# Kernel tuning notes

Hardware: AMD Instinct MI355X
Metric: run time of the kernel (lower is better)

Reference implementation:

```python
import jax, jax.numpy as jnp
import numpy as np

B, X_DIM, Y_DIM, T, LAT, H1, CH = 4096, 128, 64, 200, 100, 100, 50


def setup_inputs() -> dict:
    key = jax.random.key(0)
    ks = jax.random.split(key, 16)

    def rn(k, shape, scale):
        return (jax.random.normal(k, shape) * scale).astype(jnp.float32)

    def lin(k, fin, fout):
        # weight stored [in, out] so forward is x @ W + b (same math as torch Linear)
        return rn(k, (fin, fout), 1.0 / np.sqrt(fin)), jnp.zeros((fout,), jnp.float32)

    Wmu1, bmu1 = lin(ks[0], X_DIM, H1)
    Wmu2, bmu2 = lin(ks[1], H1, LAT)
    Wsig1, bsig1 = lin(ks[2], X_DIM, H1)
    Wsig2, bsig2 = lin(ks[3], H1, LAT)
    Wih, bih = lin(ks[4], 2 * Y_DIM, 3 * LAT)   # GRUCell input weights (r|z|n)
    Whh, bhh = lin(ks[5], LAT, 3 * LAT)          # GRUCell hidden weights (r|z|n)
    Wl1, bl1 = lin(ks[6], LAT, LAT)
    Wl2, bl2 = lin(ks[7], LAT, Y_DIM)
    Wc1, bc1 = lin(ks[8], LAT, CH)
    Wc2, bc2 = lin(ks[9], CH, 1)

    return dict(
        x=jax.random.normal(ks[10], (B, X_DIM), jnp.float32),
        y=jax.random.normal(ks[11], (B, Y_DIM, T), jnp.float32),
        y_mask=jax.random.bernoulli(ks[12], 0.5, (B, Y_DIM, T)),
        Wmu1=Wmu1, bmu1=bmu1, Wmu2=Wmu2, bmu2=bmu2,
        Wsig1=Wsig1, bsig1=bsig1, Wsig2=Wsig2, bsig2=bsig2,
        Wih=Wih, bih=bih, Whh=Whh, bhh=bhh,
        Wl1=Wl1, bl1=bl1, Wl2=Wl2, bl2=bl2,
        Wc1=Wc1, bc1=bc1, Wc2=Wc2, bc2=bc2,
    )


def reference(x, y, y_mask,
              Wmu1, bmu1, Wmu2, bmu2,
              Wsig1, bsig1, Wsig2, bsig2,
              Wih, bih, Whh, bhh,
              Wl1, bl1, Wl2, bl2,
              Wc1, bc1, Wc2, bc2):
    Bb, ydim, Tt = y.shape
    # initial hidden state: eval-mode reparametrize returns mu (log_std unused)
    mu0 = jnp.tanh(x @ Wmu1 + bmu1) @ Wmu2 + bmu2          # [B, LAT]
    h0 = mu0

    y_seq = jnp.moveaxis(y, 2, 0)                            # [T, B, ydim]
    m_seq = jnp.moveaxis(y_mask, 2, 0)                       # [T, B, ydim] bool

    def step(carry, tm):
        h, y_prev = carry
        y_t, m_t = tm
        # teacher forcing: observed entries from y, rest from previous prediction
        y_in = jnp.where(m_t, y_t, y_prev)                   # [B, ydim]
        mf = m_t.astype(h.dtype)
        # interleave (value, mask) per feature -> [B, 2*ydim]
        x_il = jnp.stack([y_in, mf], axis=2).reshape(Bb, 2 * ydim)
        gx = x_il @ Wih + bih                                # [B, 3*LAT]
        gh = h @ Whh + bhh
        gx_r, gx_z, gx_n = jnp.split(gx, 3, axis=1)
        gh_r, gh_z, gh_n = jnp.split(gh, 3, axis=1)
        r = jax.nn.sigmoid(gx_r + gh_r)
        z = jax.nn.sigmoid(gx_z + gh_z)
        n = jnp.tanh(gx_n + r * gh_n)
        h_new = (1.0 - z) * n + z * h                        # torch GRUCell update
        out_t = jnp.tanh(h_new @ Wl1 + bl1) @ Wl2 + bl2      # [B, ydim]
        return (h_new, out_t), out_t

    init = (h0, jnp.zeros((Bb, ydim), h0.dtype))
    (h_T, _), outs = jax.lax.scan(step, init, (y_seq, m_seq))
    output = jnp.moveaxis(outs, 0, 2)                        # [B, ydim, T]
    out_class = jax.nn.sigmoid(jax.nn.relu(h_T @ Wc1 + bc1) @ Wc2 + bc2)[:, 0]
    return output, out_class
```

## Files before the change

### kernel.cpp

```cpp
#include <hip/hip_runtime.h>
#include <hip/hip_bf16.h>


#define BSZ   4096
#define XD    128
#define YD    64
#define TT    200
#define NH3   300
#define RPB   16
#define NBLK  (BSZ / RPB)

typedef unsigned short u16;
typedef unsigned int   u32;
typedef __attribute__((ext_vector_type(8))) short s16x8;
typedef __attribute__((ext_vector_type(4))) float f32x4;

__device__ __forceinline__ float bf_lo(u32 u){ return __uint_as_float(u << 16); }
__device__ __forceinline__ float bf_hi(u32 u){ return __uint_as_float(u & 0xFFFF0000u); }
__device__ __forceinline__ u16 f2bf(float f){
  u32 u = __float_as_uint(f);
  u32 r = (u + 0x7FFFu + ((u >> 16) & 1u)) >> 16;
  return (u16)r;
}
__device__ __forceinline__ float loadf(const void* p, size_t i, int fmode){
  return (fmode == 0) ? __uint_as_float(((u32)((const u16*)p)[i]) << 16)
                      : ((const float*)p)[i];
}
__device__ __forceinline__ float fsig(float x){ return 1.f/(1.f + __expf(-x)); }
__device__ __forceinline__ float ftanh(float x){ float e = __expf(2.f*x); return 1.f - 2.f/(e + 1.f); }

__device__ __forceinline__ f32x4 mfma16(uint4 a, uint4 b, f32x4 c){
  s16x8 as, bs;
  __builtin_memcpy(&as, &a, 16);
  __builtin_memcpy(&bs, &b, 16);
  return __builtin_amdgcn_mfma_f32_16x16x32_bf16(as, bs, c, 0, 0, 0);
}

__device__ __forceinline__ float dotblk(const float* xr, const u16* wb, int n, int N, int KB){
  float a = 0.f;
  const uint4* wp = (const uint4*)wb;
  #pragma unroll
  for (int kb = 0; kb < KB; ++kb){
    uint4 u = wp[kb * N + n];
    const float4* xp = (const float4*)(xr + (kb << 3));
    float4 x0 = xp[0], x1 = xp[1];
    a += x0.x*bf_lo(u.x) + x0.y*bf_hi(u.x) + x0.z*bf_lo(u.y) + x0.w*bf_hi(u.y);
    a += x1.x*bf_lo(u.z) + x1.y*bf_hi(u.z) + x1.z*bf_lo(u.w) + x1.w*bf_hi(u.w);
  }
  return a;
}

__global__ void detect_kernel(const void* mask, const void* x, int* flags){
  __shared__ int cnt[4];
  if (threadIdx.x < 4) cnt[threadIdx.x] = 0;
  __syncthreads();
  if (blockIdx.x == 0){
    const unsigned char* p = (const unsigned char*)mask;
    int c0=0, c1=0, c2=0, c3=0;
    for (int i = threadIdx.x; i < 4096; i += 256){
      unsigned char b = p[i];
      if (b == 0x3F && (i & 3) == 1) c0++;
      if (b == 0x3F && (i & 3) == 3) c1++;
      if (b == 1    && (i & 3) != 0) c2++;
      if (b == 1)                    c3++;
    }
    atomicAdd(&cnt[0], c0); atomicAdd(&cnt[1], c1);
    atomicAdd(&cnt[2], c2); atomicAdd(&cnt[3], c3);
    __syncthreads();
    if (threadIdx.x == 0){
      int mm;
      if      (cnt[0] > 0) mm = 0;
      else if (cnt[1] > 0) mm = 1;
      else if (cnt[2] > 0) mm = 3;
      else if (cnt[3] > 0) mm = 2;
      else                 mm = 0;
      flags[1] = mm;
    }
  } else {
    const u16* u = (const u16*)x;
    int c = 0;
    for (int i = threadIdx.x; i < 4096; i += 256){
      int ex = (u[i] >> 7) & 0xFF;
      if (ex >= 147) c++;
    }
    atomicAdd(&cnt[0], c);
    __syncthreads();
    if (threadIdx.x == 0) flags[0] = (cnt[0] > 32) ? 1 : 0;
  }
}

struct WtP { const void* src[3]; u16* dst[3]; const int* flags; };

__global__ void wtrans_kernel(WtP a){
  const int Ks[3]  = {128, 100, 100};
  const int Ns[3]  = {100, 100,  50};
  const int KBs[3] = { 16,  13,  13};
  int m   = blockIdx.x >> 3;
  int sub = blockIdx.x & 7;
  int K = Ks[m], N = Ns[m], KB = KBs[m];
  const void* src = a.src[m];
  u16* dst = a.dst[m];
  int fmode = a.flags[0];
  int E = KB * N * 8;
  for (int e = sub*256 + threadIdx.x; e < E; e += 8*256){
    int idx = e >> 3, kc = e & 7;
    int n = idx % N, kb = idx / N;
    int k = kb*8 + kc;
    float v = (k < K) ? loadf(src, (size_t)k * N + n, fmode) : 0.f;
    dst[e] = f2bf(v);
  }
}

struct FrP { const void* src[4]; u16* dst[4]; const int* flags; };

__global__ void fragk(FrP a){
  const int Ks[4]  = {128, 100, 100, 100};
  const int Ns[4]  = {300, 300, 100,  64};
  const int NTs[4] = { 20,  20,   8,   4};
  int m   = blockIdx.x >> 3;
  int sub = blockIdx.x & 7;
  int K = Ks[m], N = Ns[m];
  const void* src = a.src[m];
  u16* dst = a.dst[m];
  int fmode = a.flags[0];
  int E = NTs[m] * 2048;
  for (int e = sub*256 + threadIdx.x; e < E; e += 8*256){
    int j    = e & 7;
    int lane = (e >> 3) & 63;
    int kc   = (e >> 9) & 3;
    int nt   = e >> 11;
    int k = kc*32 + ((lane >> 4) << 3) + j;
    int n = nt*16 + (lane & 15);
    float v = (k < K && n < N) ? loadf(src, (size_t)k * N + n, fmode) : 0.f;
    dst[e] = f2bf(v);
  }
}

struct MainP {
  const void *x, *y, *mask;
  const void *bmu1, *bmu2, *bih, *bhh, *bl1, *bl2, *bc1, *bc2, *wc2;
  const u16 *Wmu1b, *Wmu2b, *Wc1b;
  const u16 *fih, *fhh, *fl1, *fl2;
  const int* flags;
  void* out;
};

__device__ __forceinline__ void load_win8(const void* Y, const void* M, int row0, int t,
                                          int fmode, int mmode, uint4* yv, u32& mb){
  mb = 0u;
  #pragma unroll
  for (int p = 0; p < 4; ++p){
    int idx = threadIdx.x + (p << 8);
    int r = idx >> 6, d = idx & 63;
    size_t base = ((size_t)(row0 + r)*64 + d)*200 + t;
    uint4 yw;
    if (fmode == 0){
      yw = *(const uint4*)((const u16*)Y + base);
    } else {
      const float* yf = (const float*)Y + base;
      float4 f0 = *(const float4*)yf;
      float4 f1 = *(const float4*)(yf + 4);
      yw.x = (u32)f2bf(f0.x) | ((u32)f2bf(f0.y) << 16);
      yw.y = (u32)f2bf(f0.z) | ((u32)f2bf(f0.w) << 16);
      yw.z = (u32)f2bf(f1.x) | ((u32)f2bf(f1.y) << 16);
      yw.w = (u32)f2bf(f1.z) | ((u32)f2bf(f1.w) << 16);
    }
    yv[p] = yw;
    u32 bits = 0;
    if (mmode == 0){
      uint4 mw = *(const uint4*)((const u16*)M + base);
      u32 w0 = mw.x, w1 = mw.y, w2 = mw.z, w3 = mw.w;
      if (w0 & 0xFFFFu) bits |= 1u;  if (w0 >> 16) bits |= 2u;
      if (w1 & 0xFFFFu) bits |= 4u;  if (w1 >> 16) bits |= 8u;
      if (w2 & 0xFFFFu) bits |= 16u; if (w2 >> 16) bits |= 32u;
      if (w3 & 0xFFFFu) bits |= 64u; if (w3 >> 16) bits |= 128u;
    } else if (mmode == 1){
      const float* mf = (const float*)M + base;
      float4 f0 = *(const float4*)mf;
      float4 f1 = *(const float4*)(mf + 4);
      if (f0.x != 0.f) bits |= 1u;  if (f0.y != 0.f) bits |= 2u;
      if (f0.z != 0.f) bits |= 4u;  if (f0.w != 0.f) bits |= 8u;
      if (f1.x != 0.f) bits |= 16u; if (f1.y != 0.f) bits |= 32u;
      if (f1.z != 0.f) bits |= 64u; if (f1.w != 0.f) bits |= 128u;
    } else if (mmode == 2){
      const int* mi = (const int*)M + base;
      int4 v0 = *(const int4*)mi;
      int4 v1 = *(const int4*)(mi + 4);
      if (v0.x) bits |= 1u;  if (v0.y) bits |= 2u;
      if (v0.z) bits |= 4u;  if (v0.w) bits |= 8u;
      if (v1.x) bits |= 16u; if (v1.y) bits |= 32u;
      if (v1.z) bits |= 64u; if (v1.w) bits |= 128u;
    } else {
      uint2 u = *(const uint2*)((const unsigned char*)M + base);
      #pragma unroll
      for (int q = 0; q < 4; ++q){
        if ((u.x >> (q*8)) & 0xFFu) bits |= 1u << q;
        if ((u.y >> (q*8)) & 0xFFu) bits |= 1u << (4 + q);
      }
    }
    mb |= bits << (p << 3);
  }
}

__global__ __launch_bounds__(256, 1) void gru_main(MainP P){
  __shared__ u16   XIL[RPB*136];
  __shared__ u16   HB [RPB*136];
  __shared__ u16   HN2[RPB*136];
  __shared__ float HF [RPB*108];
  __shared__ float SRZ[RPB*204];
  __shared__ float GXN[RPB*108];
  __shared__ float GHN[RPB*108];
  __shared__ u16   OS [RPB*64*16];
  __shared__ float BIH[304], BHH[304], BL1[128], BL2[64], BC1[64], WC2[64], BMU1[112], BMU2[112];

  const int tid  = threadIdx.x;
  const int row0 = blockIdx.x * RPB;
  const int fmode = P.flags[0];
  const int mmode = P.flags[1];
  const int w  = tid >> 6;
  const int ln = tid & 63;
  const int col = ln & 15;
  const int q4  = (ln >> 4) << 2;

  uint4 yc[4], yn[4];
  u32 mc, mn;
  load_win8(P.y, P.mask, row0, 0, fmode, mmode, yc, mc);
  load_win8(P.y, P.mask, row0, 8, fmode, mmode, yn, mn);

  uint4 wih[5][4], whh[5][4], wl1[2][4], wl2[4];
  #pragma unroll
  for (int i = 0; i < 5; ++i){
    int nt = w + 4*i;
    #pragma unroll
    for (int kc = 0; kc < 4; ++kc){
      wih[i][kc] = *(const uint4*)(P.fih + (((nt*4 + kc) << 6) + ln)*8);
      whh[i][kc] = *(const uint4*)(P.fhh + (((nt*4 + kc) << 6) + ln)*8);
    }
  }
  #pragma unroll
  for (int i = 0; i < 2; ++i){
    int nt = w + 4*i;
    #pragma unroll
    for (int kc = 0; kc < 4; ++kc)
      wl1[i][kc] = *(const uint4*)(P.fl1 + (((nt*4 + kc) << 6) + ln)*8);
  }
  #pragma unroll
  for (int kc = 0; kc < 4; ++kc)
    wl2[kc] = *(const uint4*)(P.fl2 + (((w*4 + kc) << 6) + ln)*8);

  for (int i = tid; i < RPB*136/2; i += 256){ ((u32*)HB)[i] = 0u; ((u32*)HN2)[i] = 0u; }
  for (int i = tid; i < RPB*108;   i += 256){ HF[i] = 0.f; GXN[i] = 0.f; GHN[i] = 0.f; }
  for (int i = tid; i < RPB*64*8;  i += 256){ ((u32*)OS)[i] = 0u; }

  for (int i = tid; i < 304; i += 256){
    BIH[i] = (i < 300) ? loadf(P.bih, i, fmode) : 0.f;
    BHH[i] = (i < 300) ? loadf(P.bhh, i, fmode) : 0.f;
  }
  if (tid < 128) BL1[tid] = (tid < 100) ? loadf(P.bl1, tid, fmode) : 0.f;
  if (tid < 64){
    BL2[tid] = loadf(P.bl2, tid, fmode);
    BC1[tid] = (tid < 50) ? loadf(P.bc1, tid, fmode) : 0.f;
    WC2[tid] = (tid < 50) ? loadf(P.wc2, tid, fmode) : 0.f;
  }
  if (tid < 112){
    BMU1[tid] = (tid < 100) ? loadf(P.bmu1, tid, fmode) : 0.f;
    BMU2[tid] = (tid < 100) ? loadf(P.bmu2, tid, fmode) : 0.f;
  }
  __syncthreads();

  #pragma unroll
  for (int p = 0; p < 2; ++p){
    int idx = tid + (p << 8);
    int r = idx >> 5, kq = idx & 31;
    size_t base = ((size_t)(row0 + r) << 7) + ((size_t)kq << 2);
    float v0, v1, v2, v3;
    if (fmode == 0){
      uint2 u = *(const uint2*)((const u16*)P.x + base);
      v0 = bf_lo(u.x); v1 = bf_hi(u.x); v2 = bf_lo(u.y); v3 = bf_hi(u.y);
    } else {
      float4 f = *(const float4*)((const float*)P.x + base);
      v0 = f.x; v1 = f.y; v2 = f.z; v3 = f.w;
    }
    float* dst = &SRZ[r*204 + (kq << 2)];
    dst[0] = v0; dst[1] = v1; dst[2] = v2; dst[3] = v3;
  }
  __syncthreads();
  for (int p = 0; p < 7; ++p){
    int idx = tid + (p << 8);
    if (idx < RPB*100){
      int r = idx / 100, j = idx - r*100;
      GXN[r*108 + j] = ftanh(BMU1[j] + dotblk(&SRZ[r*204], P.Wmu1b, j, 100, 16));
    }
  }
  __syncthreads();
  for (int p = 0; p < 7; ++p){
    int idx = tid + (p << 8);
    if (idx < RPB*100){
      int r = idx / 100, j = idx - r*100;
      float hv = BMU2[j] + dotblk(&GXN[r*108], P.Wmu2b, j, 100, 13);
      HF[r*108 + j] = hv;
      HB[r*136 + j] = f2bf(hv);
    }
  }
  __syncthreads();

  for (int t = 0; t < TT; ++t){
    const int tc8 = t & 7;

    if (tc8 == 0 && t){
      #pragma unroll
      for (int p = 0; p < 4; ++p) yc[p] = yn[p];
      mc = mn;
      if (t + 8 < TT) load_win8(P.y, P.mask, row0, t + 8, fmode, mmode, yn, mn);
    }
    if ((t & 15) == 0 && t){
      int t0 = t - 16;
      #pragma unroll
      for (int p = 0; p < 4; ++p){
        int idx = tid + (p << 8);
        int r = idx >> 6, d = idx & 63;
        size_t base = ((size_t)(row0 + r)*64 + d)*200 + t0;
        const uint4* po = (const uint4*)&OS[(r*64 + d)*16];
        if (fmode == 0){
          u16* ob = (u16*)P.out + base;
          *(uint4*)ob = po[0];
          *(uint4*)(ob + 8) = po[1];
        } else {
          float* of = (float*)P.out + base;
          uint4 a = po[0], b = po[1];
          float4 f0 = {bf_lo(a.x), bf_hi(a.x), bf_lo(a.y), bf_hi(a.y)};
          float4 f1 = {bf_lo(a.z), bf_hi(a.z), bf_lo(a.w), bf_hi(a.w)};
          float4 f2 = {bf_lo(b.x), bf_hi(b.x), bf_lo(b.y), bf_hi(b.y)};
          float4 f3 = {bf_lo(b.z), bf_hi(b.z), bf_lo(b.w), bf_hi(b.w)};
          *(float4*)of = f0; *(float4*)(of+4) = f1;
          *(float4*)(of+8) = f2; *(float4*)(of+12) = f3;
        }
      }
    }

    #pragma unroll
    for (int p = 0; p < 4; ++p){
      int idx = tid + (p << 8);
      int r = idx >> 6, d = idx & 63;
      u32 w01 = (tc8 & 2) ? yc[p].y : yc[p].x;
      u32 w23 = (tc8 & 2) ? yc[p].w : yc[p].z;
      u32 word = (tc8 & 4) ? w23 : w01;
      u16 yv16 = (tc8 & 1) ? (u16)(word >> 16) : (u16)(word & 0xFFFFu);
      bool mv = (mc >> ((p << 3) | tc8)) & 1u;
      u16 yp16 = OS[(r*64 + d)*16 + ((t + 15) & 15)];
      u32 val = (u32)(mv ? yv16 : yp16) | ((mv ? 0x3F80u : 0u) << 16);
      *(u32*)(&XIL[r*136 + (d << 1)]) = val;
    }
    __syncthreads();

    {
      uint4 xa[4], ha[4];
      #pragma unroll
      for (int kc = 0; kc < 4; ++kc){
        int ao = (ln & 15)*136 + kc*32 + ((ln >> 4) << 3);
        xa[kc] = *(const uint4*)(&XIL[ao]);
        ha[kc] = *(const uint4*)(&HB[ao]);
      }
      #pragma unroll
      for (int i = 0; i < 3; ++i){
        f32x4 ac = {0.f, 0.f, 0.f, 0.f};
        #pragma unroll
        for (int kc = 0; kc < 4; ++kc) ac = mfma16(xa[kc], wih[i][kc], ac);
        #pragma unroll
        for (int kc = 0; kc < 4; ++kc) ac = mfma16(ha[kc], whh[i][kc], ac);
        int n = (w + 4*i)*16 + col;
        float bb = BIH[n] + BHH[n];
        #pragma unroll
        for (int reg = 0; reg < 4; ++reg)
          SRZ[(q4 + reg)*204 + n] = ac[reg] + bb;
      }
      #pragma unroll
      for (int i = 3; i < 5; ++i){
        f32x4 ax = {0.f,0.f,0.f,0.f}, ah = {0.f,0.f,0.f,0.f};
        #pragma unroll
        for (int kc = 0; kc < 4; ++kc){
          ax = mfma16(xa[kc], wih[i][kc], ax);
          ah = mfma16(ha[kc], whh[i][kc], ah);
        }
        int n = (w + 4*i)*16 + col;
        if (n < 200){
          float bb = BIH[n] + BHH[n];
          #pragma unroll
          for (int reg = 0; reg < 4; ++reg)
            SRZ[(q4 + reg)*204 + n] = ax[reg] + ah[reg] + bb;
        } else if (n < 304){
          float b1 = BIH[n], b2 = BHH[n];
          #pragma unroll
          for (int reg = 0; reg < 4; ++reg){
            GXN[(q4 + reg)*108 + n - 200] = ax[reg] + b1;
            GHN[(q4 + reg)*108 + n - 200] = ah[reg] + b2;
          }
        }
      }
    }
    __syncthreads();

    for (int p = 0; p < 7; ++p){
      int idx = tid + (p << 8);
      if (idx < RPB*100){
        int r = idx / 100, j = idx - r*100;
        float rr = fsig(SRZ[r*204 + j]);
        float zz = fsig(SRZ[r*204 + 100 + j]);
        float nn = ftanh(GXN[r*108 + j] + rr*GHN[r*108 + j]);
        float hv = (1.f - zz)*nn + zz*HF[r*108 + j];
        HF[r*108 + j] = hv;
        HB[r*136 + j] = f2bf(hv);
      }
    }
    __syncthreads();

    {
      uint4 ha[4];
      #pragma unroll
      for (int kc = 0; kc < 4; ++kc){
        int ao = (ln & 15)*136 + kc*32 + ((ln >> 4) << 3);
        ha[kc] = *(const uint4*)(&HB[ao]);
      }
      #pragma unroll
      for (int i = 0; i < 2; ++i){
        f32x4 ac = {0.f,0.f,0.f,0.f};
        #pragma unroll
        for (int kc = 0; kc < 4; ++kc) ac = mfma16(ha[kc], wl1[i][kc], ac);
        int n = (w + 4*i)*16 + col;
        #pragma unroll
        for (int reg = 0; reg < 4; ++reg)
          HN2[(q4 + reg)*136 + n] = f2bf(ftanh(ac[reg] + BL1[n]));
      }
    }
    __syncthreads();

    {
      uint4 na[4];
      #pragma unroll
      for (int kc = 0; kc < 4; ++kc){
        int ao = (ln & 15)*136 + kc*32 + ((ln >> 4) << 3);
        na[kc] = *(const uint4*)(&HN2[ao]);
      }
      f32x4 ac = {0.f,0.f,0.f,0.f};
      #pragma unroll
      for (int kc = 0; kc < 4; ++kc) ac = mfma16(na[kc], wl2[kc], ac);
      int d = w*16 + col;
      #pragma unroll
      for (int reg = 0; reg < 4; ++reg){
        float o = ac[reg] + BL2[d];
        OS[((q4 + reg)*64 + d)*16 + (t & 15)] = f2bf(o);
      }
    }
    __syncthreads();
  }

  {
    int t0 = TT - 8;
    #pragma unroll
    for (int p = 0; p < 4; ++p){
      int idx = tid + (p << 8);
      int r = idx >> 6, d = idx & 63;
      size_t base = ((size_t)(row0 + r)*64 + d)*200 + t0;
      const uint4* po = (const uint4*)&OS[(r*64 + d)*16];
      if (fmode == 0){
        *(uint4*)((u16*)P.out + base) = po[0];
      } else {
        float* of = (float*)P.out + base;
        uint4 a = po[0];
        float4 f0 = {bf_lo(a.x), bf_hi(a.x), bf_lo(a.y), bf_hi(a.y)};
        float4 f1 = {bf_lo(a.z), bf_hi(a.z), bf_lo(a.w), bf_hi(a.w)};
        *(float4*)of = f0; *(float4*)(of+4) = f1;
      }
    }
  }

  for (int p = 0; p < 4; ++p){
    int idx = tid + (p << 8);
    if (idx < RPB*50){
      int r = idx / 50, j = idx - r*50;
      float c = BC1[j] + dotblk(&HF[r*108], P.Wc1b, j, 50, 13);
      GXN[r*108 + j] = fmaxf(c, 0.f);
    }
  }
  __syncthreads();
  if (tid < RPB){
    float oc = loadf(P.bc2, 0, fmode);
    for (int j = 0; j < 50; ++j) oc += GXN[tid*108 + j]*WC2[j];
    float sg = fsig(oc);
    size_t off = (size_t)BSZ*YD*TT + row0 + tid;
    if (fmode == 0) ((u16*)P.out)[off] = f2bf(sg);
    else            ((float*)P.out)[off] = sg;
  }
}

extern "C" void kernel_launch(void* const* d_in, const int* in_sizes, int n_in,
                              void* d_out, int out_size, void* d_ws, size_t ws_size,
                              hipStream_t stream){
  int* flags = (int*)d_ws;
  u16* wb = (u16*)((char*)d_ws + 256);
  u16* Wmu1b = wb;
  u16* Wmu2b = wb + 12800;
  u16* Wc1b  = wb + 23200;
  u16* fih   = wb + 28400;
  u16* fhh   = wb + 69360;
  u16* fl1   = wb + 110320;
  u16* fl2   = wb + 126704;

  detect_kernel<<<2, 256, 0, stream>>>(d_in[2], d_in[0], flags);

  WtP wp;
  wp.flags = flags;
  wp.src[0] = d_in[3];  wp.dst[0] = Wmu1b;
  wp.src[1] = d_in[5];  wp.dst[1] = Wmu2b;
  wp.src[2] = d_in[19]; wp.dst[2] = Wc1b;
  wtrans_kernel<<<24, 256, 0, stream>>>(wp);

  FrP fp;
  fp.flags = flags;
  fp.src[0] = d_in[11]; fp.dst[0] = fih;
  fp.src[1] = d_in[13]; fp.dst[1] = fhh;
  fp.src[2] = d_in[15]; fp.dst[2] = fl1;
  fp.src[3] = d_in[17]; fp.dst[3] = fl2;
  fragk<<<32, 256, 0, stream>>>(fp);

  MainP mp;
  mp.x = d_in[0]; mp.y = d_in[1]; mp.mask = d_in[2];
  mp.bmu1 = d_in[4];  mp.bmu2 = d_in[6];
  mp.bih  = d_in[12]; mp.bhh  = d_in[14];
  mp.bl1  = d_in[16]; mp.bl2  = d_in[18];
  mp.bc1  = d_in[20]; mp.bc2  = d_in[22]; mp.wc2 = d_in[21];
  mp.Wmu1b = Wmu1b; mp.Wmu2b = Wmu2b; mp.Wc1b = Wc1b;
  mp.fih = fih; mp.fhh = fhh; mp.fl1 = fl1; mp.fl2 = fl2;
  mp.flags = flags; mp.out = d_out;
  gru_main<<<NBLK, 256, 0, stream>>>(mp);
}
```

Measured before the change: 1.491 ms.

## Halve rows per block, keep hidden state in registers, swizzle output staging buffer

Cuts rows per block from 16 to 8, doubling the block count to 512, and allows two blocks per CU so more waves can hide the per-step barrier and latency stalls. MFMA tiles still cover 16 rows, so half the lanes compute padding rows that are masked on writeback. The fp32 hidden state now lives in registers across timesteps instead of shared memory. The output staging buffer gets an XOR swizzle to reduce LDS bank conflicts. The cost is wasted MFMA work on the padding rows and more register pressure under the tighter launch bound.

```diff
diff --git a/kernel.cpp b/kernel.cpp
--- a/kernel.cpp
+++ b/kernel.cpp
@@ -7,7 +7,7 @@
 #define YD    64
 #define TT    200
 #define NH3   300
-#define RPB   16
+#define RPB   8
 #define NBLK  (BSZ / RPB)
 
 typedef unsigned short u16;
@@ -149,7 +149,7 @@
                                           int fmode, int mmode, uint4* yv, u32& mb){
   mb = 0u;
   #pragma unroll
-  for (int p = 0; p < 4; ++p){
+  for (int p = 0; p < 2; ++p){
     int idx = threadIdx.x + (p << 8);
     int r = idx >> 6, d = idx & 63;
     size_t base = ((size_t)(row0 + r)*64 + d)*200 + t;
@@ -202,10 +202,10 @@
   }
 }
 
-__global__ __launch_bounds__(256, 1) void gru_main(MainP P){
-  __shared__ u16   XIL[RPB*136];
-  __shared__ u16   HB [RPB*136];
-  __shared__ u16   HN2[RPB*136];
+__global__ __launch_bounds__(256, 2) void gru_main(MainP P){
+  __shared__ u16   XIL[16*136];
+  __shared__ u16   HB [16*136];
+  __shared__ u16   HN2[16*136];
   __shared__ float HF [RPB*108];
   __shared__ float SRZ[RPB*204];
   __shared__ float GXN[RPB*108];
@@ -222,7 +222,7 @@
   const int col = ln & 15;
   const int q4  = (ln >> 4) << 2;
 
-  uint4 yc[4], yn[4];
+  uint4 yc[2], yn[2];
   u32 mc, mn;
   load_win8(P.y, P.mask, row0, 0, fmode, mmode, yc, mc);
   load_win8(P.y, P.mask, row0, 8, fmode, mmode, yn, mn);
@@ -248,9 +248,11 @@
   for (int kc = 0; kc < 4; ++kc)
     wl2[kc] = *(const uint4*)(P.fl2 + (((w*4 + kc) << 6) + ln)*8);
 
-  for (int i = tid; i < RPB*136/2; i += 256){ ((u32*)HB)[i] = 0u; ((u32*)HN2)[i] = 0u; }
-  for (int i = tid; i < RPB*108;   i += 256){ HF[i] = 0.f; GXN[i] = 0.f; GHN[i] = 0.f; }
-  for (int i = tid; i < RPB*64*8;  i += 256){ ((u32*)OS)[i] = 0u; }
+  for (int i = tid; i < 16*136/2; i += 256){
+    ((u32*)XIL)[i] = 0u; ((u32*)HB)[i] = 0u; ((u32*)HN2)[i] = 0u;
+  }
+  for (int i = tid; i < RPB*108; i += 256){ HF[i] = 0.f; GXN[i] = 0.f; GHN[i] = 0.f; }
+  for (int i = tid; i < RPB*64*8; i += 256){ ((u32*)OS)[i] = 0u; }
 
   for (int i = tid; i < 304; i += 256){
     BIH[i] = (i < 300) ? loadf(P.bih, i, fmode) : 0.f;
@@ -268,9 +270,8 @@
   }
   __syncthreads();
 
-  #pragma unroll
-  for (int p = 0; p < 2; ++p){
-    int idx = tid + (p << 8);
+  {
+    int idx = tid;
     int r = idx >> 5, kq = idx & 31;
     size_t base = ((size_t)(row0 + r) << 7) + ((size_t)kq << 2);
     float v0, v1, v2, v3;
@@ -285,7 +286,8 @@
     dst[0] = v0; dst[1] = v1; dst[2] = v2; dst[3] = v3;
   }
   __syncthreads();
-  for (int p = 0; p < 7; ++p){
+  #pragma unroll
+  for (int p = 0; p < 4; ++p){
     int idx = tid + (p << 8);
     if (idx < RPB*100){
       int r = idx / 100, j = idx - r*100;
@@ -293,12 +295,14 @@
     }
   }
   __syncthreads();
-  for (int p = 0; p < 7; ++p){
+  float hreg[4];
+  #pragma unroll
+  for (int p = 0; p < 4; ++p){
     int idx = tid + (p << 8);
     if (idx < RPB*100){
       int r = idx / 100, j = idx - r*100;
       float hv = BMU2[j] + dotblk(&GXN[r*108], P.Wmu2b, j, 100, 13);
-      HF[r*108 + j] = hv;
+      hreg[p] = hv;
       HB[r*136 + j] = f2bf(hv);
     }
   }
@@ -309,29 +313,36 @@
 
     if (tc8 == 0 && t){
       #pragma unroll
-      for (int p = 0; p < 4; ++p) yc[p] = yn[p];
+      for (int p = 0; p < 2; ++p) yc[p] = yn[p];
       mc = mn;
       if (t + 8 < TT) load_win8(P.y, P.mask, row0, t + 8, fmode, mmode, yn, mn);
     }
     if ((t & 15) == 0 && t){
       int t0 = t - 16;
-      #pragma unroll
-      for (int p = 0; p < 4; ++p){
+      const u32* ow = (const u32*)OS;
+      #pragma unroll
+      for (int p = 0; p < 2; ++p){
         int idx = tid + (p << 8);
         int r = idx >> 6, d = idx & 63;
+        int swz = ((d >> 2) ^ r) & 7;
+        int wb = idx << 3;
+        u32 w0 = ow[wb + (0 ^ swz)], w1 = ow[wb + (1 ^ swz)];
+        u32 w2 = ow[wb + (2 ^ swz)], w3 = ow[wb + (3 ^ swz)];
+        u32 w4 = ow[wb + (4 ^ swz)], w5 = ow[wb + (5 ^ swz)];
+        u32 w6 = ow[wb + (6 ^ swz)], w7 = ow[wb + (7 ^ swz)];
         size_t base = ((size_t)(row0 + r)*64 + d)*200 + t0;
-        const uint4* po = (const uint4*)&OS[(r*64 + d)*16];
         if (fmode == 0){
           u16* ob = (u16*)P.out + base;
-          *(uint4*)ob = po[0];
-          *(uint4*)(ob + 8) = po[1];
+          uint4 a; a.x = w0; a.y = w1; a.z = w2; a.w = w3;
+          uint4 b; b.x = w4; b.y = w5; b.z = w6; b.w = w7;
+          *(uint4*)ob = a;
+          *(uint4*)(ob + 8) = b;
         } else {
           float* of = (float*)P.out + base;
-          uint4 a = po[0], b = po[1];
-          float4 f0 = {bf_lo(a.x), bf_hi(a.x), bf_lo(a.y), bf_hi(a.y)};
-          float4 f1 = {bf_lo(a.z), bf_hi(a.z), bf_lo(a.w), bf_hi(a.w)};
-          float4 f2 = {bf_lo(b.x), bf_hi(b.x), bf_lo(b.y), bf_hi(b.y)};
-          float4 f3 = {bf_lo(b.z), bf_hi(b.z), bf_lo(b.w), bf_hi(b.w)};
+          float4 f0 = {bf_lo(w0), bf_hi(w0), bf_lo(w1), bf_hi(w1)};
+          float4 f1 = {bf_lo(w2), bf_hi(w2), bf_lo(w3), bf_hi(w3)};
+          float4 f2 = {bf_lo(w4), bf_hi(w4), bf_lo(w5), bf_hi(w5)};
+          float4 f3 = {bf_lo(w6), bf_hi(w6), bf_lo(w7), bf_hi(w7)};
           *(float4*)of = f0; *(float4*)(of+4) = f1;
           *(float4*)(of+8) = f2; *(float4*)(of+12) = f3;
         }
@@ -339,7 +350,7 @@
     }
 
     #pragma unroll
-    for (int p = 0; p < 4; ++p){
+    for (int p = 0; p < 2; ++p){
       int idx = tid + (p << 8);
       int r = idx >> 6, d = idx & 63;
       u32 w01 = (tc8 & 2) ? yc[p].y : yc[p].x;
@@ -347,7 +358,8 @@
       u32 word = (tc8 & 4) ? w23 : w01;
       u16 yv16 = (tc8 & 1) ? (u16)(word >> 16) : (u16)(word & 0xFFFFu);
       bool mv = (mc >> ((p << 3) | tc8)) & 1u;
-      u16 yp16 = OS[(r*64 + d)*16 + ((t + 15) & 15)];
+      int sl = ((t + 15) & 15) ^ ((((d >> 2) ^ r) & 7) << 1);
+      u16 yp16 = OS[(idx << 4) + sl];
       u32 val = (u32)(mv ? yv16 : yp16) | ((mv ? 0x3F80u : 0u) << 16);
       *(u32*)(&XIL[r*136 + (d << 1)]) = val;
     }
@@ -368,11 +380,13 @@
         for (int kc = 0; kc < 4; ++kc) ac = mfma16(xa[kc], wih[i][kc], ac);
         #pragma unroll
         for (int kc = 0; kc < 4; ++kc) ac = mfma16(ha[kc], whh[i][kc], ac);
-        int n = (w + 4*i)*16 + col;
-        float bb = BIH[n] + BHH[n];
-        #pragma unroll
-        for (int reg = 0; reg < 4; ++reg)
-          SRZ[(q4 + reg)*204 + n] = ac[reg] + bb;
+        if (ln < 32){
+          int n = (w + 4*i)*16 + col;
+          float bb = BIH[n] + BHH[n];
+          #pragma unroll
+          for (int reg = 0; reg < 4; ++reg)
+            SRZ[(q4 + reg)*204 + n] = ac[reg] + bb;
+        }
       }
       #pragma unroll
       for (int i = 3; i < 5; ++i){
@@ -382,33 +396,36 @@
           ax = mfma16(xa[kc], wih[i][kc], ax);
           ah = mfma16(ha[kc], whh[i][kc], ah);
         }
-        int n = (w + 4*i)*16 + col;
-        if (n < 200){
-          float bb = BIH[n] + BHH[n];
-          #pragma unroll
-          for (int reg = 0; reg < 4; ++reg)
-            SRZ[(q4 + reg)*204 + n] = ax[reg] + ah[reg] + bb;
-        } else if (n < 304){
-          float b1 = BIH[n], b2 = BHH[n];
-          #pragma unroll
-          for (int reg = 0; reg < 4; ++reg){
-            GXN[(q4 + reg)*108 + n - 200] = ax[reg] + b1;
-            GHN[(q4 + reg)*108 + n - 200] = ah[reg] + b2;
+        if (ln < 32){
+          int n = (w + 4*i)*16 + col;
+          if (n < 200){
+            float bb = BIH[n] + BHH[n];
+            #pragma unroll
+            for (int reg = 0; reg < 4; ++reg)
+              SRZ[(q4 + reg)*204 + n] = ax[reg] + ah[reg] + bb;
+          } else if (n < 304){
+            float b1 = BIH[n], b2 = BHH[n];
+            #pragma unroll
+            for (int reg = 0; reg < 4; ++reg){
+              GXN[(q4 + reg)*108 + n - 200] = ax[reg] + b1;
+              GHN[(q4 + reg)*108 + n - 200] = ah[reg] + b2;
+            }
           }
         }
       }
     }
     __syncthreads();
 
-    for (int p = 0; p < 7; ++p){
+    #pragma unroll
+    for (int p = 0; p < 4; ++p){
       int idx = tid + (p << 8);
       if (idx < RPB*100){
         int r = idx / 100, j = idx - r*100;
         float rr = fsig(SRZ[r*204 + j]);
         float zz = fsig(SRZ[r*204 + 100 + j]);
         float nn = ftanh(GXN[r*108 + j] + rr*GHN[r*108 + j]);
-        float hv = (1.f - zz)*nn + zz*HF[r*108 + j];
-        HF[r*108 + j] = hv;
+        float hv = (1.f - zz)*nn + zz*hreg[p];
+        hreg[p] = hv;
         HB[r*136 + j] = f2bf(hv);
       }
     }
@@ -426,10 +443,12 @@
         f32x4 ac = {0.f,0.f,0.f,0.f};
         #pragma unroll
         for (int kc = 0; kc < 4; ++kc) ac = mfma16(ha[kc], wl1[i][kc], ac);
-        int n = (w + 4*i)*16 + col;
-        #pragma unroll
-        for (int reg = 0; reg < 4; ++reg)
-          HN2[(q4 + reg)*136 + n] = f2bf(ftanh(ac[reg] + BL1[n]));
+        if (ln < 32){
+          int n = (w + 4*i)*16 + col;
+          #pragma unroll
+          for (int reg = 0; reg < 4; ++reg)
+            HN2[(q4 + reg)*136 + n] = f2bf(ftanh(ac[reg] + BL1[n]));
+        }
       }
     }
     __syncthreads();
@@ -444,11 +463,15 @@
       f32x4 ac = {0.f,0.f,0.f,0.f};
       #pragma unroll
       for (int kc = 0; kc < 4; ++kc) ac = mfma16(na[kc], wl2[kc], ac);
-      int d = w*16 + col;
-      #pragma unroll
-      for (int reg = 0; reg < 4; ++reg){
-        float o = ac[reg] + BL2[d];
-        OS[((q4 + reg)*64 + d)*16 + (t & 15)] = f2bf(o);
+      if (ln < 32){
+        int d = w*16 + col;
+        #pragma unroll
+        for (int reg = 0; reg < 4; ++reg){
+          float o = ac[reg] + BL2[d];
+          int rr = q4 + reg;
+          int sl = (t & 15) ^ ((((d >> 2) ^ rr) & 7) << 1);
+          OS[((rr*64 + d) << 4) + sl] = f2bf(o);
+        }
       }
     }
     __syncthreads();
@@ -456,25 +479,40 @@
 
   {
     int t0 = TT - 8;
+    const u32* ow = (const u32*)OS;
     #pragma unroll
-    for (int p = 0; p < 4; ++p){
+    for (int p = 0; p < 2; ++p){
       int idx = tid + (p << 8);
       int r = idx >> 6, d = idx & 63;
+      int swz = ((d >> 2) ^ r) & 7;
+      int wb = idx << 3;
+      u32 w0 = ow[wb + (0 ^ swz)], w1 = ow[wb + (1 ^ swz)];
+      u32 w2 = ow[wb + (2 ^ swz)], w3 = ow[wb + (3 ^ swz)];
       size_t base = ((size_t)(row0 + r)*64 + d)*200 + t0;
-      const uint4* po = (const uint4*)&OS[(r*64 + d)*16];
       if (fmode == 0){
-        *(uint4*)((u16*)P.out + base) = po[0];
+        uint4 a; a.x = w0; a.y = w1; a.z = w2; a.w = w3;
+        *(uint4*)((u16*)P.out + base) = a;
       } else {
         float* of = (float*)P.out + base;
-        uint4 a = po[0];
-        float4 f0 = {bf_lo(a.x), bf_hi(a.x), bf_lo(a.y), bf_hi(a.y)};
-        float4 f1 = {bf_lo(a.z), bf_hi(a.z), bf_lo(a.w), bf_hi(a.w)};
+        float4 f0 = {bf_lo(w0), bf_hi(w0), bf_lo(w1), bf_hi(w1)};
+        float4 f1 = {bf_lo(w2), bf_hi(w2), bf_lo(w3), bf_hi(w3)};
         *(float4*)of = f0; *(float4*)(of+4) = f1;
       }
     }
   }
 
+  #pragma unroll
   for (int p = 0; p < 4; ++p){
+    int idx = tid + (p << 8);
+    if (idx < RPB*100){
+      int r = idx / 100, j = idx - r*100;
+      HF[r*108 + j] = hreg[p];
+    }
+  }
+  __syncthreads();
+
+  #pragma unroll
+  for (int p = 0; p < 2; ++p){
     int idx = tid + (p << 8);
     if (idx < RPB*50){
       int r = idx / 50, j = idx - r*50;
```

Result: slower. 2.827 ms (+89.6%).
